# Performance work log

Hardware: AMD Instinct MI355X
Metric: run time of the kernel (lower is better)

Reference implementation:

```python
import jax, jax.numpy as jnp
import numpy as np

INPUT_SIZE = 1024
HIDDEN_SIZE = 1024
BATCH = 32
SEQ = 512


def setup_inputs() -> dict:
    key = jax.random.key(0)
    ks = jax.random.split(key, 20)
    stdv = 1.0 / np.sqrt(HIDDEN_SIZE)

    def u(k, shape):
        return jax.random.uniform(k, shape, jnp.float32, -stdv, stdv)

    inp = {
        'inputs': jax.random.normal(ks[0], (BATCH, SEQ, INPUT_SIZE), jnp.float32),
        'h0': jax.random.normal(ks[1], (1, BATCH, HIDDEN_SIZE), jnp.float32),
        'c0': jax.random.normal(ks[2], (1, BATCH, HIDDEN_SIZE), jnp.float32),
    }
    names = ['ii', 'hi', 'if_', 'hf', 'io', 'ho', 'ig', 'hg']
    kidx = 3
    for n in names:
        in_dim = INPUT_SIZE if n[0] == 'i' and n not in ('hi', 'hf', 'ho', 'hg') else HIDDEN_SIZE
        inp['w_' + n] = u(ks[kidx], (HIDDEN_SIZE, in_dim)); kidx += 1
        inp['b_' + n] = u(ks[kidx], (HIDDEN_SIZE, 1)); kidx += 1
    return inp


def _gate(x, h0s, w_i, b_i, w_h, b_h):
    # x: [B,T,I]; h0s: [B,H]; w_i: [H,I]; w_h: [H,H]; biases [H,1]
    z = (jnp.einsum('bti,hi->bth', x, w_i)
         + (h0s @ w_h.T)[:, None, :]
         + b_i[:, 0] + b_h[:, 0])
    return z


def reference(inputs, h0, c0,
              w_ii, b_ii, w_hi, b_hi,
              w_if_, b_if_, w_hf, b_hf,
              w_io, b_io, w_ho, b_ho,
              w_ig, b_ig, w_hg, b_hg):
    # Faithful to source: h_t/c_t are NEVER updated inside the time loop
    # (original code omits the reassignment), so all timesteps use the
    # initial state -> fully vectorizable over T.
    h0s = h0[0]  # [B,H]
    c0s = c0[0]  # [B,H]
    i = jax.nn.sigmoid(_gate(inputs, h0s, w_ii, b_ii, w_hi, b_hi))
    f = jax.nn.sigmoid(_gate(inputs, h0s, w_if_, b_if_, w_hf, b_hf))
    g = jnp.tanh(_gate(inputs, h0s, w_ig, b_ig, w_hg, b_hg))
    o = jax.nn.sigmoid(_gate(inputs, h0s, w_io, b_io, w_ho, b_ho))
    c_next = f * c0s[:, None, :] + i * g          # [B,T,H]
    h_next = o * jnp.tanh(c_next)                 # [B,T,H]
    hidden_seq = jnp.transpose(h_next, (1, 0, 2))  # [T,B,H] (torch cat over dim 0)
    h_last = hidden_seq[-1][None]                  # [1,B,H]
    c_last = c_next[:, -1][None]                   # [1,B,H]
    return hidden_seq, h_last, c_last
```

## Files before the change

kernel.cpp:

```cpp
#include <hip/hip_runtime.h>
#include <hip/hip_bf16.h>

#define HSEQ 16777216
#define NH 1024

typedef __attribute__((ext_vector_type(8))) short bf16x8;
typedef __attribute__((ext_vector_type(4))) float f32x4;

__device__ __forceinline__ unsigned short f2bf(float f) {
  unsigned u = __builtin_bit_cast(unsigned, f);
  u += 0x7fffu + ((u >> 16) & 1u);
  return (unsigned short)(u >> 16);
}

__device__ __forceinline__ float fsig(float z) {
  float e = __builtin_amdgcn_exp2f(-1.442695041f * z);
  return __builtin_amdgcn_rcpf(1.f + e);
}
__device__ __forceinline__ float ftanh(float z) {
  float e = __builtin_amdgcn_exp2f(2.885390082f * z);
  return 1.f - 2.f * __builtin_amdgcn_rcpf(1.f + e);
}

__global__ __launch_bounds__(256) void cvt_all(
    const float* __restrict__ x,
    const float* __restrict__ wi, const float* __restrict__ wf,
    const float* __restrict__ wo, const float* __restrict__ wg,
    unsigned short* __restrict__ xb, unsigned short* __restrict__ wb) {
  int bid = blockIdx.x;
  const float* src; unsigned short* dst; int base, iters;
  if (bid < 2048) {
    src = x; dst = xb; base = bid * 8192; iters = 8;
  } else {
    int g = bid - 2048; int ws = g >> 8; int blk = g & 255;
    src = (ws == 0) ? wi : (ws == 1) ? wf : (ws == 2) ? wo : wg;
    dst = wb + ws * 1048576; base = blk * 4096; iters = 4;
  }
  int t = threadIdx.x;
  for (int i = 0; i < iters; ++i) {
    int idx = base + i * 1024 + t * 4;
    float4 v = *reinterpret_cast<const float4*>(src + idx);
    ushort4 o;
    o.x = f2bf(v.x); o.y = f2bf(v.y); o.z = f2bf(v.z); o.w = f2bf(v.w);
    *reinterpret_cast<ushort4*>(dst + idx) = o;
  }
}

__global__ __launch_bounds__(256) void hz_kernel(
    const float* __restrict__ h0,
    const float* __restrict__ wh_i, const float* __restrict__ wh_f,
    const float* __restrict__ wh_o, const float* __restrict__ wh_g,
    const float* __restrict__ bi_i, const float* __restrict__ bh_i,
    const float* __restrict__ bi_f, const float* __restrict__ bh_f,
    const float* __restrict__ bi_o, const float* __restrict__ bh_o,
    const float* __restrict__ bi_g, const float* __restrict__ bh_g,
    float* __restrict__ hz) {
  __shared__ float ws[8 * 1024];
  int g = blockIdx.x >> 7;
  int hb = blockIdx.x & 127;
  const float* wh = (g == 0) ? wh_i : (g == 1) ? wh_f : (g == 2) ? wh_o : wh_g;
  const float* bi = (g == 0) ? bi_i : (g == 1) ? bi_f : (g == 2) ? bi_o : bi_g;
  const float* bh = (g == 0) ? bh_i : (g == 1) ? bh_f : (g == 2) ? bh_o : bh_g;
  int tid = threadIdx.x;
  const float4* wsrc = reinterpret_cast<const float4*>(wh + hb * 8 * 1024);
  float4* wdst = reinterpret_cast<float4*>(ws);
  for (int i = tid; i < 2048; i += 256) wdst[i] = wsrc[i];
  __syncthreads();
  int b = tid & 31;
  int hh = tid >> 5;
  const float4* hv = reinterpret_cast<const float4*>(h0 + b * NH);
  const float4* wv = reinterpret_cast<const float4*>(ws + hh * NH);
  float acc = 0.f;
  for (int k = 0; k < 256; ++k) {
    float4 a = hv[k], w4 = wv[k];
    acc += a.x * w4.x + a.y * w4.y + a.z * w4.z + a.w * w4.w;
  }
  int h = hb * 8 + hh;
  hz[g * (32 * NH) + b * NH + h] = acc + bi[h] + bh[h];
}

__device__ __forceinline__ void load_lds16(const void* gsrc, void* lds) {
  __builtin_amdgcn_global_load_lds(
      (const __attribute__((address_space(1))) unsigned int*)gsrc,
      (__attribute__((address_space(3))) unsigned int*)lds, 16, 0, 0);
}

__global__ __launch_bounds__(256, 4) void lstm_gemm(
    const unsigned short* __restrict__ xb,
    const unsigned short* __restrict__ wb,
    const float* __restrict__ hz,
    const float* __restrict__ c0,
    float* __restrict__ out) {
  __shared__ unsigned short As[128 * 64];
  __shared__ unsigned short Bs[128 * 64];

  const int orig = blockIdx.x;
  const int xcd = orig & 7;
  const int local = orig >> 3;
  const int mt = (xcd >> 1) * 32 + (local >> 4);
  const int ht = (xcd & 1) * 16 + (local & 15);
  const int mBase = mt * 128;
  const int hBase = ht * 32;

  const int tid = threadIdx.x;
  const int lane = tid & 63;
  const int w = tid >> 6;
  const int laneLow = lane & 15;
  const int lane4 = lane >> 4;

  const int sR = lane >> 3;
  const int sL = ((lane & 7) ^ sR) * 8;

  f32x4 acc[2][8];
#pragma unroll
  for (int i = 0; i < 2; ++i)
#pragma unroll
    for (int j = 0; j < 8; ++j) acc[i][j] = (f32x4){0.f, 0.f, 0.f, 0.f};

  for (int kt = 0; kt < 16; ++kt) {
    const int k0 = kt * 64;
#pragma unroll
    for (int j = 0; j < 4; ++j) {
      int c = j * 4 + w;
      int row = c * 8 + sR;
      load_lds16(xb + (size_t)(mBase + row) * 1024 + k0 + sL, As + c * 512);
    }
#pragma unroll
    for (int j = 0; j < 4; ++j) {
      int c = j * 4 + w;
      int n = c * 8 + sR;
      int gate = n >> 5, hh = n & 31;
      load_lds16(wb + (size_t)gate * 1048576 + (size_t)(hBase + hh) * 1024 + k0 + sL,
                 Bs + c * 512);
    }
    asm volatile("s_waitcnt vmcnt(0)" ::: "memory");
    __builtin_amdgcn_s_barrier();

    bf16x8 af[2][2];
#pragma unroll
    for (int mi = 0; mi < 2; ++mi)
#pragma unroll
      for (int kk = 0; kk < 2; ++kk) {
        int row = w * 32 + mi * 16 + laneLow;
        int slot = (kk * 4 + lane4) ^ (laneLow & 7);
        af[mi][kk] = *reinterpret_cast<const bf16x8*>(&As[row * 64 + slot * 8]);
      }
#pragma unroll
    for (int nf = 0; nf < 8; ++nf) {
      bf16x8 bfb0, bfb1;
      {
        int n = nf * 16 + laneLow;
        int slot0 = (0 * 4 + lane4) ^ (laneLow & 7);
        int slot1 = (1 * 4 + lane4) ^ (laneLow & 7);
        bfb0 = *reinterpret_cast<const bf16x8*>(&Bs[n * 64 + slot0 * 8]);
        bfb1 = *reinterpret_cast<const bf16x8*>(&Bs[n * 64 + slot1 * 8]);
      }
      acc[0][nf] = __builtin_amdgcn_mfma_f32_16x16x32_bf16(af[0][0], bfb0, acc[0][nf], 0, 0, 0);
      acc[1][nf] = __builtin_amdgcn_mfma_f32_16x16x32_bf16(af[1][0], bfb0, acc[1][nf], 0, 0, 0);
      acc[0][nf] = __builtin_amdgcn_mfma_f32_16x16x32_bf16(af[0][1], bfb1, acc[0][nf], 0, 0, 0);
      acc[1][nf] = __builtin_amdgcn_mfma_f32_16x16x32_bf16(af[1][1], bfb1, acc[1][nf], 0, 0, 0);
    }
    __builtin_amdgcn_s_barrier();
  }

  const int b = mBase >> 9;
#pragma unroll
  for (int mi = 0; mi < 2; ++mi) {
#pragma unroll
    for (int n16 = 0; n16 < 2; ++n16) {
      int h = hBase + n16 * 16 + laneLow;
      float hz_i = hz[0 * 32768 + b * NH + h];
      float hz_f = hz[1 * 32768 + b * NH + h];
      float hz_o = hz[2 * 32768 + b * NH + h];
      float hz_g = hz[3 * 32768 + b * NH + h];
      float c0v = c0[b * NH + h];
#pragma unroll
      for (int r = 0; r < 4; ++r) {
        int row = w * 32 + mi * 16 + lane4 * 4 + r;
        int m = mBase + row;
        int t = m & 511;
        float zi = acc[mi][0 + n16][r] + hz_i;
        float zf = acc[mi][2 + n16][r] + hz_f;
        float zo = acc[mi][4 + n16][r] + hz_o;
        float zg = acc[mi][6 + n16][r] + hz_g;
        float iv = fsig(zi);
        float fv = fsig(zf);
        float ov = fsig(zo);
        float gv = ftanh(zg);
        float cv = fv * c0v + iv * gv;
        float hval = ov * ftanh(cv);
        out[((size_t)t * 32 + b) * 1024 + h] = hval;
        if (t == 511) {
          out[HSEQ + b * NH + h] = hval;
          out[HSEQ + 32768 + b * NH + h] = cv;
        }
      }
    }
  }
}

extern "C" void kernel_launch(void* const* d_in, const int* in_sizes, int n_in,
                              void* d_out, int out_size, void* d_ws, size_t ws_size,
                              hipStream_t stream) {
  const float* x    = (const float*)d_in[0];
  const float* h0   = (const float*)d_in[1];
  const float* c0   = (const float*)d_in[2];
  const float* w_ii = (const float*)d_in[3];
  const float* b_ii = (const float*)d_in[4];
  const float* w_hi = (const float*)d_in[5];
  const float* b_hi = (const float*)d_in[6];
  const float* w_if = (const float*)d_in[7];
  const float* b_if = (const float*)d_in[8];
  const float* w_hf = (const float*)d_in[9];
  const float* b_hf = (const float*)d_in[10];
  const float* w_io = (const float*)d_in[11];
  const float* b_io = (const float*)d_in[12];
  const float* w_ho = (const float*)d_in[13];
  const float* b_ho = (const float*)d_in[14];
  const float* w_ig = (const float*)d_in[15];
  const float* b_ig = (const float*)d_in[16];
  const float* w_hg = (const float*)d_in[17];
  const float* b_hg = (const float*)d_in[18];

  unsigned short* xb = (unsigned short*)d_ws;
  unsigned short* wb = xb + 16777216;
  float* hz = (float*)(wb + 4 * 1048576);
  float* out = (float*)d_out;

  hipLaunchKernelGGL(cvt_all, dim3(3072), dim3(256), 0, stream,
                     x, w_ii, w_if, w_io, w_ig, xb, wb);
  hipLaunchKernelGGL(hz_kernel, dim3(512), dim3(256), 0, stream, h0,
                     w_hi, w_hf, w_ho, w_hg,
                     b_ii, b_hi, b_if, b_hf, b_io, b_ho, b_ig, b_hg, hz);
  hipLaunchKernelGGL(lstm_gemm, dim3(4096), dim3(256), 0, stream, xb, wb, hz, c0, out);
}
```

Before: 206.4 us.

## Fuse input fp32-to-bf16 conversion into GEMM loads and merge prep kernels

Drops the separate pass that converted the input activations to bf16. The GEMM now loads fp32 input directly into registers, converts to bf16 and writes it into LDS, and the weight conversion and h0 projection are merged into one launch. This avoids writing and re-reading a 32 MB bf16 copy of the input and removes one kernel launch. The cost is that each GEMM tile reads twice the bytes for the A operand, and the conversion work is repeated across the 32 h-tiles that share the same rows. The A loads become synchronous register loads instead of async loads to LDS.

```diff
diff --git a/kernel.cpp b/kernel.cpp
--- a/kernel.cpp
+++ b/kernel.cpp
@@ -22,31 +22,10 @@
   return 1.f - 2.f * __builtin_amdgcn_rcpf(1.f + e);
 }
 
-__global__ __launch_bounds__(256) void cvt_all(
-    const float* __restrict__ x,
+__global__ __launch_bounds__(256) void cvt_w_hz(
     const float* __restrict__ wi, const float* __restrict__ wf,
     const float* __restrict__ wo, const float* __restrict__ wg,
-    unsigned short* __restrict__ xb, unsigned short* __restrict__ wb) {
-  int bid = blockIdx.x;
-  const float* src; unsigned short* dst; int base, iters;
-  if (bid < 2048) {
-    src = x; dst = xb; base = bid * 8192; iters = 8;
-  } else {
-    int g = bid - 2048; int ws = g >> 8; int blk = g & 255;
-    src = (ws == 0) ? wi : (ws == 1) ? wf : (ws == 2) ? wo : wg;
-    dst = wb + ws * 1048576; base = blk * 4096; iters = 4;
-  }
-  int t = threadIdx.x;
-  for (int i = 0; i < iters; ++i) {
-    int idx = base + i * 1024 + t * 4;
-    float4 v = *reinterpret_cast<const float4*>(src + idx);
-    ushort4 o;
-    o.x = f2bf(v.x); o.y = f2bf(v.y); o.z = f2bf(v.z); o.w = f2bf(v.w);
-    *reinterpret_cast<ushort4*>(dst + idx) = o;
-  }
-}
-
-__global__ __launch_bounds__(256) void hz_kernel(
+    unsigned short* __restrict__ wb,
     const float* __restrict__ h0,
     const float* __restrict__ wh_i, const float* __restrict__ wh_f,
     const float* __restrict__ wh_o, const float* __restrict__ wh_g,
@@ -55,28 +34,44 @@
     const float* __restrict__ bi_o, const float* __restrict__ bh_o,
     const float* __restrict__ bi_g, const float* __restrict__ bh_g,
     float* __restrict__ hz) {
-  __shared__ float ws[8 * 1024];
-  int g = blockIdx.x >> 7;
-  int hb = blockIdx.x & 127;
-  const float* wh = (g == 0) ? wh_i : (g == 1) ? wh_f : (g == 2) ? wh_o : wh_g;
-  const float* bi = (g == 0) ? bi_i : (g == 1) ? bi_f : (g == 2) ? bi_o : bi_g;
-  const float* bh = (g == 0) ? bh_i : (g == 1) ? bh_f : (g == 2) ? bh_o : bh_g;
+  int bid = blockIdx.x;
   int tid = threadIdx.x;
-  const float4* wsrc = reinterpret_cast<const float4*>(wh + hb * 8 * 1024);
-  float4* wdst = reinterpret_cast<float4*>(ws);
-  for (int i = tid; i < 2048; i += 256) wdst[i] = wsrc[i];
-  __syncthreads();
-  int b = tid & 31;
-  int hh = tid >> 5;
-  const float4* hv = reinterpret_cast<const float4*>(h0 + b * NH);
-  const float4* wv = reinterpret_cast<const float4*>(ws + hh * NH);
-  float acc = 0.f;
-  for (int k = 0; k < 256; ++k) {
-    float4 a = hv[k], w4 = wv[k];
-    acc += a.x * w4.x + a.y * w4.y + a.z * w4.z + a.w * w4.w;
+  if (bid < 1024) {
+    int ws = bid >> 8, blk = bid & 255;
+    const float* src = (ws == 0) ? wi : (ws == 1) ? wf : (ws == 2) ? wo : wg;
+    unsigned short* dst = wb + ws * 1048576;
+    int base = blk * 4096;
+    for (int i = 0; i < 4; ++i) {
+      int idx = base + i * 1024 + tid * 4;
+      float4 v = *reinterpret_cast<const float4*>(src + idx);
+      ushort4 o;
+      o.x = f2bf(v.x); o.y = f2bf(v.y); o.z = f2bf(v.z); o.w = f2bf(v.w);
+      *reinterpret_cast<ushort4*>(dst + idx) = o;
+    }
+  } else {
+    __shared__ float ws[8 * 1024];
+    int hbid = bid - 1024;
+    int g = hbid >> 7;
+    int hb = hbid & 127;
+    const float* wh = (g == 0) ? wh_i : (g == 1) ? wh_f : (g == 2) ? wh_o : wh_g;
+    const float* bi = (g == 0) ? bi_i : (g == 1) ? bi_f : (g == 2) ? bi_o : bi_g;
+    const float* bh = (g == 0) ? bh_i : (g == 1) ? bh_f : (g == 2) ? bh_o : bh_g;
+    const float4* wsrc = reinterpret_cast<const float4*>(wh + hb * 8 * 1024);
+    float4* wdst = reinterpret_cast<float4*>(ws);
+    for (int i = tid; i < 2048; i += 256) wdst[i] = wsrc[i];
+    __syncthreads();
+    int b = tid & 31;
+    int hh = tid >> 5;
+    const float4* hv = reinterpret_cast<const float4*>(h0 + b * NH);
+    const float4* wv = reinterpret_cast<const float4*>(ws + hh * NH);
+    float acc = 0.f;
+    for (int k = 0; k < 256; ++k) {
+      float4 a = hv[k], w4 = wv[k];
+      acc += a.x * w4.x + a.y * w4.y + a.z * w4.z + a.w * w4.w;
+    }
+    int h = hb * 8 + hh;
+    hz[g * (32 * NH) + b * NH + h] = acc + bi[h] + bh[h];
   }
-  int h = hb * 8 + hh;
-  hz[g * (32 * NH) + b * NH + h] = acc + bi[h] + bh[h];
 }
 
 __device__ __forceinline__ void load_lds16(const void* gsrc, void* lds) {
@@ -86,7 +81,7 @@
 }
 
 __global__ __launch_bounds__(256, 4) void lstm_gemm(
-    const unsigned short* __restrict__ xb,
+    const float* __restrict__ x,
     const unsigned short* __restrict__ wb,
     const float* __restrict__ hz,
     const float* __restrict__ c0,
@@ -119,11 +114,13 @@
 
   for (int kt = 0; kt < 16; ++kt) {
     const int k0 = kt * 64;
+    float4 a0[4], a1[4];
 #pragma unroll
     for (int j = 0; j < 4; ++j) {
       int c = j * 4 + w;
-      int row = c * 8 + sR;
-      load_lds16(xb + (size_t)(mBase + row) * 1024 + k0 + sL, As + c * 512);
+      const float* src = x + (size_t)(mBase + c * 8 + sR) * 1024 + k0 + sL;
+      a0[j] = *reinterpret_cast<const float4*>(src);
+      a1[j] = *reinterpret_cast<const float4*>(src + 4);
     }
 #pragma unroll
     for (int j = 0; j < 4; ++j) {
@@ -133,8 +130,17 @@
       load_lds16(wb + (size_t)gate * 1048576 + (size_t)(hBase + hh) * 1024 + k0 + sL,
                  Bs + c * 512);
     }
-    asm volatile("s_waitcnt vmcnt(0)" ::: "memory");
-    __builtin_amdgcn_s_barrier();
+#pragma unroll
+    for (int j = 0; j < 4; ++j) {
+      int c = j * 4 + w;
+      bf16x8 v;
+      v[0] = (short)f2bf(a0[j].x); v[1] = (short)f2bf(a0[j].y);
+      v[2] = (short)f2bf(a0[j].z); v[3] = (short)f2bf(a0[j].w);
+      v[4] = (short)f2bf(a1[j].x); v[5] = (short)f2bf(a1[j].y);
+      v[6] = (short)f2bf(a1[j].z); v[7] = (short)f2bf(a1[j].w);
+      *reinterpret_cast<bf16x8*>(&As[c * 512 + lane * 8]) = v;
+    }
+    __syncthreads();
 
     bf16x8 af[2][2];
 #pragma unroll
@@ -160,7 +166,7 @@
       acc[0][nf] = __builtin_amdgcn_mfma_f32_16x16x32_bf16(af[0][1], bfb1, acc[0][nf], 0, 0, 0);
       acc[1][nf] = __builtin_amdgcn_mfma_f32_16x16x32_bf16(af[1][1], bfb1, acc[1][nf], 0, 0, 0);
     }
-    __builtin_amdgcn_s_barrier();
+    __syncthreads();
   }
 
   const int b = mBase >> 9;
@@ -222,15 +228,13 @@
   const float* w_hg = (const float*)d_in[17];
   const float* b_hg = (const float*)d_in[18];
 
-  unsigned short* xb = (unsigned short*)d_ws;
-  unsigned short* wb = xb + 16777216;
+  unsigned short* wb = (unsigned short*)d_ws;
   float* hz = (float*)(wb + 4 * 1048576);
   float* out = (float*)d_out;
 
-  hipLaunchKernelGGL(cvt_all, dim3(3072), dim3(256), 0, stream,
-                     x, w_ii, w_if, w_io, w_ig, xb, wb);
-  hipLaunchKernelGGL(hz_kernel, dim3(512), dim3(256), 0, stream, h0,
-                     w_hi, w_hf, w_ho, w_hg,
+  hipLaunchKernelGGL(cvt_w_hz, dim3(1536), dim3(256), 0, stream,
+                     w_ii, w_if, w_io, w_ig, wb,
+                     h0, w_hi, w_hf, w_ho, w_hg,
                      b_ii, b_hi, b_if, b_hf, b_io, b_ho, b_ig, b_hg, hz);
-  hipLaunchKernelGGL(lstm_gemm, dim3(4096), dim3(256), 0, stream, xb, wb, hz, c0, out);
-}
+  hipLaunchKernelGGL(lstm_gemm, dim3(4096), dim3(256), 0, stream, x, wb, hz, c0, out);
+}
```

After: 295.2 us. 1.43x slower.
